# Kernel optimization log

Measured on AMD Instinct MI355X. Metric: run time of the kernel, lower is better.

Reference implementation:

```python
import jax, jax.numpy as jnp
import numpy as np

B, T, C, H, E = 4, 128, 256, 8, 64  # batch, tokens, n_embd, n_head, edge_dim
D = C // H


def setup_inputs() -> dict:
    key = jax.random.key(0)
    ks = jax.random.split(key, 12)
    s = 0.02
    return {
        "x": jax.random.normal(ks[0], (B, T, C), jnp.float32),
        "aux_x": jax.random.normal(ks[1], (B, T, C), jnp.float32),
        "mask": jnp.ones((B, T, T), jnp.int32),
        "edge": jax.random.normal(ks[2], (B, T, T, E), jnp.float32),
        "Wq": jax.random.normal(ks[3], (C, C), jnp.float32) * s,
        "bq": jnp.zeros((C,), jnp.float32),
        "Wk": jax.random.normal(ks[4], (C, C + E), jnp.float32) * s,
        "bk": jnp.zeros((C,), jnp.float32),
        "Wv": jax.random.normal(ks[5], (C, C + E), jnp.float32) * s,
        "bv": jnp.zeros((C,), jnp.float32),
        "Wp": jax.random.normal(ks[6], (C, C), jnp.float32) * s,
        "bp": jnp.zeros((C,), jnp.float32),
    }


def reference(x, aux_x, mask, edge, Wq, bq, Wk, bk, Wv, bv, Wp, bp):
    Bx, Tx, Cx = x.shape
    q = x @ Wq.T + bq  # [B,T,C]
    # per-pair augmented features: node i broadcast over all j, concat edge(i,j)
    aug = jnp.concatenate(
        [jnp.broadcast_to(x[:, :, None, :], (Bx, Tx, Tx, Cx)), edge], axis=-1
    )  # [B,T,T,C+E]
    k = aug @ Wk.T + bk  # [B,T,T,C]
    v = aug @ Wv.T + bv  # [B,T,T,C]
    q = q.reshape(Bx, Tx, H, D).transpose(0, 2, 1, 3)          # [B,H,T,D]
    k = k.reshape(Bx, Tx, Tx, H, D).transpose(0, 3, 1, 2, 4)   # [B,H,T,T,D]
    v = v.reshape(Bx, Tx, Tx, H, D).transpose(0, 3, 1, 2, 4)   # [B,H,T,T,D]
    att = jnp.einsum('bhid,bhijd->bhij', q, k) * (1.0 / jnp.sqrt(jnp.float32(D)))
    att = jnp.where(mask[:, None] == 0, -jnp.inf, att)
    all_masked = (mask == 0).all(-1)[:, None, :, None]  # rows with no valid key
    att = jnp.where(all_masked, 0.0, att)
    fi = jnp.finfo(att.dtype)
    att = jnp.nan_to_num(att, nan=0.0, posinf=fi.max, neginf=fi.min)
    att = jax.nn.softmax(att, axis=-1)
    y = jnp.einsum('bhij,bhijd->bhid', att, v)  # [B,H,T,D]
    y = y.transpose(0, 2, 1, 3).reshape(Bx, Tx, Cx)
    return y @ Wp.T + bp
```

## Files before the change

### kernel.cpp

```cpp
#include <hip/hip_runtime.h>

#define SENT (-3.402823466e38f)

typedef __attribute__((ext_vector_type(8))) short short8;
typedef __attribute__((ext_vector_type(4))) float floatx4;

#define OFF_QKP   0
#define OFF_AGG   131072
#define OFF_VNODE 262144

__device__ __forceinline__ ushort f2b(float f) {
    uint u = __float_as_uint(f);
    u += 0x7FFFu + ((u >> 16) & 1u);
    return (ushort)(u >> 16);
}
__device__ __forceinline__ short8 pk8(float4 a, float4 b) {
    short8 r;
    r[0]=(short)f2b(a.x); r[1]=(short)f2b(a.y); r[2]=(short)f2b(a.z); r[3]=(short)f2b(a.w);
    r[4]=(short)f2b(b.x); r[5]=(short)f2b(b.y); r[6]=(short)f2b(b.z); r[7]=(short)f2b(b.w);
    return r;
}

__global__ __launch_bounds__(256, 4)
void k1_proj(const float* __restrict__ x, const float* __restrict__ Wq,
             const float* __restrict__ Wv, const float* __restrict__ Wk,
             const float* __restrict__ bq, const float* __restrict__ bv,
             float* __restrict__ vnode, ushort* __restrict__ qkp) {
    __shared__ float xL[16][264];
    __shared__ float qls[16][66];
    int tid = threadIdx.x;
    int w = tid >> 6, lane = tid & 63, g = lane >> 4, r = lane & 15;
    int m  = blockIdx.x & 1;
    int ct = (blockIdx.x >> 1) & 3;
    int rt = blockIdx.x >> 3;
    int r0 = rt*16, c0 = ct*64;

    #pragma unroll
    for (int it = 0; it < 4; ++it) {
        int fid = (tid + 256*it)*4;
        int rr = fid >> 8, k = fid & 255;
        *(float4*)&xL[rr][k] = *(const float4*)&x[(size_t)(r0+rr)*256 + k];
    }
    __syncthreads();

    int c = c0 + w*16 + r;
    const float* Wrow = m ? (Wv + (size_t)c*320) : (Wq + (size_t)c*256);
    floatx4 acc = {0.f,0.f,0.f,0.f};
    #pragma unroll
    for (int kt = 0; kt < 8; ++kt) {
        int k0 = kt*32 + g*8;
        short8 af = pk8(*(float4*)&xL[r][k0], *(float4*)&xL[r][k0+4]);
        short8 bf = pk8(*(const float4*)&Wrow[k0], *(const float4*)&Wrow[k0+4]);
        acc = __builtin_amdgcn_mfma_f32_16x16x32_bf16(af, bf, acc, 0,0,0);
    }
    float bb = m ? bv[c] : bq[c];
    if (m) {
        #pragma unroll
        for (int i = 0; i < 4; ++i)
            vnode[(size_t)(r0 + 4*g + i)*256 + c] = acc[i] + bb;
    } else {
        #pragma unroll
        for (int i = 0; i < 4; ++i)
            qls[4*g + i][w*16 + r] = acc[i] + bb;
        __syncthreads();
        int rr = tid >> 4, es = tid & 15;
        int h0 = ct*2;
        float a0[4] = {0,0,0,0}, a1[4] = {0,0,0,0};
        const float* wk0 = Wk + (size_t)(h0*32)*320 + 256 + es*4;
        const float* wk1 = Wk + (size_t)((h0+1)*32)*320 + 256 + es*4;
        #pragma unroll 8
        for (int d = 0; d < 32; ++d) {
            float q0 = qls[rr][d];
            float q1 = qls[rr][32 + d];
            float4 w0 = *(const float4*)&wk0[(size_t)d*320];
            float4 w1 = *(const float4*)&wk1[(size_t)d*320];
            a0[0]+=q0*w0.x; a0[1]+=q0*w0.y; a0[2]+=q0*w0.z; a0[3]+=q0*w0.w;
            a1[0]+=q1*w1.x; a1[1]+=q1*w1.y; a1[2]+=q1*w1.z; a1[3]+=q1*w1.w;
        }
        const float s = 0.17677669529663687f;
        ushort4 u0, u1;
        u0.x=f2b(a0[0]*s); u0.y=f2b(a0[1]*s); u0.z=f2b(a0[2]*s); u0.w=f2b(a0[3]*s);
        u1.x=f2b(a1[0]*s); u1.y=f2b(a1[1]*s); u1.z=f2b(a1[2]*s); u1.w=f2b(a1[3]*s);
        size_t base = (size_t)(r0 + rr)*512;
        *(ushort4*)&qkp[base + h0*64 + es*4]     = u0;
        *(ushort4*)&qkp[base + (h0+1)*64 + es*4] = u1;
    }
}

__global__ __launch_bounds__(512, 4)
void k2_attn(const float* __restrict__ edge, const int* __restrict__ msk,
             const ushort* __restrict__ qkp, ushort* __restrict__ aggO) {
    __shared__ ushort edsA[128][72];
    __shared__ ushort qkpL[16][64];
    __shared__ float  attL[8][132];
    __shared__ ushort attT[16][136];
    __shared__ float  mval[128];
    int tid = threadIdx.x;
    int w = tid >> 6, lane = tid & 63, g = lane >> 4, r = lane & 15;
    int row = blockIdx.x;

    float4 ef[4];
    const float* eg = edge + (size_t)row*8192;
    #pragma unroll
    for (int it = 0; it < 4; ++it)
        ef[it] = *(const float4*)(eg + (size_t)(tid + 512*it)*4);

    if (tid < 256) {
        ushort* qf = (ushort*)qkpL;
        *(uint*)&qf[tid*2]        = *(const uint*)&qkp[(size_t)row*512 + tid*2];
        *(uint*)&qf[512 + tid*2]  = 0u;
    }
    if (tid < 128) mval[tid] = (msk[(size_t)row*128 + tid] != 0) ? 1.0f : 0.0f;
    if (tid < 136) {
        #pragma unroll
        for (int hp = 8; hp < 16; ++hp) attT[hp][tid] = 0;
    }
    #pragma unroll
    for (int it = 0; it < 4; ++it) {
        int fid = (tid + 512*it)*4;
        int j = fid >> 6, e = fid & 63;
        uint lo = (uint)f2b(ef[it].x) | ((uint)f2b(ef[it].y) << 16);
        uint hi = (uint)f2b(ef[it].z) | ((uint)f2b(ef[it].w) << 16);
        *(uint2*)&edsA[j][e] = make_uint2(lo, hi);
    }
    __syncthreads();

    {
        int mt = w;
        floatx4 acc = {0,0,0,0};
        #pragma unroll
        for (int kt = 0; kt < 2; ++kt) {
            short8 af = *(short8*)&edsA[mt*16 + r][kt*32 + g*8];
            short8 bf = *(short8*)&qkpL[r][kt*32 + g*8];
            acc = __builtin_amdgcn_mfma_f32_16x16x32_bf16(af, bf, acc, 0,0,0);
        }
        if (r < 8) {
            #pragma unroll
            for (int i = 0; i < 4; ++i) {
                int j = mt*16 + 4*g + i;
                attL[r][j] = (mval[j] > 0.5f) ? acc[i] : SENT;
            }
        }
    }
    __syncthreads();

    {
        int h = w;
        float v0 = attL[h][lane];
        float v1 = attL[h][64 + lane];
        float mx = fmaxf(v0, v1);
        #pragma unroll
        for (int off = 32; off >= 1; off >>= 1) mx = fmaxf(mx, __shfl_xor(mx, off));
        float e0 = __expf(v0 - mx), e1 = __expf(v1 - mx);
        float smv = e0 + e1;
        #pragma unroll
        for (int off = 32; off >= 1; off >>= 1) smv += __shfl_xor(smv, off);
        float inv = 1.0f / smv;
        attT[h][lane]      = f2b(e0 * inv);
        attT[h][64 + lane] = f2b(e1 * inv);
    }
    __syncthreads();

    if (w < 4) {
        floatx4 acc = {0,0,0,0};
        #pragma unroll
        for (int kt = 0; kt < 4; ++kt) {
            short8 a2 = *(short8*)&attT[r][kt*32 + g*8];
            short8 b2;
            #pragma unroll
            for (int jj = 0; jj < 8; ++jj)
                b2[jj] = (short)edsA[kt*32 + g*8 + jj][w*16 + r];
            acc = __builtin_amdgcn_mfma_f32_16x16x32_bf16(a2, b2, acc, 0,0,0);
        }
        #pragma unroll
        for (int i = 0; i < 4; ++i) {
            int h = 4*g + i;
            if (h < 8)
                aggO[(size_t)row*512 + h*64 + w*16 + r] = f2b(acc[i]);
        }
    }
}

__global__ __launch_bounds__(256, 2)
void k3_out(const float* __restrict__ vnode, const ushort* __restrict__ aggI,
            const float* __restrict__ Wv, const float* __restrict__ Wp,
            const float* __restrict__ bp, float* __restrict__ out) {
    __shared__ ushort yL[16][264];
    int tid = threadIdx.x;
    int w = tid >> 6, lane = tid & 63, g = lane >> 4, r = lane & 15;
    int rt = blockIdx.x >> 2, ob = blockIdx.x & 3;
    int r0 = rt*16, o0 = ob*64;

    {
        #pragma unroll
        for (int pi = 0; pi < 4; ++pi) {
            int p = w*4 + pi, h = p >> 1, ntl = p & 1;
            int c = h*32 + ntl*16 + r;
            floatx4 acc;
            #pragma unroll
            for (int i = 0; i < 4; ++i)
                acc[i] = vnode[(size_t)(r0 + 4*g + i)*256 + c];
            #pragma unroll
            for (int kt = 0; kt < 2; ++kt) {
                short8 af = *(const short8*)&aggI[(size_t)(r0 + r)*512 + h*64 + kt*32 + g*8];
                const float* wr = Wv + (size_t)c*320 + 256 + kt*32 + g*8;
                short8 bf = pk8(*(const float4*)wr, *(const float4*)(wr + 4));
                acc = __builtin_amdgcn_mfma_f32_16x16x32_bf16(af, bf, acc, 0,0,0);
            }
            #pragma unroll
            for (int i = 0; i < 4; ++i)
                yL[4*g + i][c] = f2b(acc[i]);
        }
    }
    __syncthreads();

    {
        int o = o0 + w*16 + r;
        floatx4 acc = {0,0,0,0};
        const float* wr = Wp + (size_t)o*256;
        #pragma unroll
        for (int kt = 0; kt < 8; ++kt) {
            int k0 = kt*32 + g*8;
            short8 af = *(short8*)&yL[r][k0];
            short8 bf = pk8(*(const float4*)&wr[k0], *(const float4*)&wr[k0+4]);
            acc = __builtin_amdgcn_mfma_f32_16x16x32_bf16(af, bf, acc, 0,0,0);
        }
        float bb = bp[o];
        #pragma unroll
        for (int i = 0; i < 4; ++i)
            out[(size_t)(r0 + 4*g + i)*256 + o] = acc[i] + bb;
    }
}

extern "C" void kernel_launch(void* const* d_in, const int* in_sizes, int n_in,
                              void* d_out, int out_size, void* d_ws, size_t ws_size,
                              hipStream_t stream) {
    (void)in_sizes; (void)n_in; (void)out_size; (void)ws_size;
    const float* x    = (const float*)d_in[0];
    const int*   msk  = (const int*)d_in[2];
    const float* edge = (const float*)d_in[3];
    const float* Wq   = (const float*)d_in[4];
    const float* bq   = (const float*)d_in[5];
    const float* Wk   = (const float*)d_in[6];
    const float* Wv   = (const float*)d_in[8];
    const float* bv   = (const float*)d_in[9];
    const float* Wp   = (const float*)d_in[10];
    const float* bp   = (const float*)d_in[11];
    float* out = (float*)d_out;
    float* ws  = (float*)d_ws;

    ushort* qkp   = (ushort*)(ws + OFF_QKP);
    ushort* agg   = (ushort*)(ws + OFF_AGG);
    float*  vnode = ws + OFF_VNODE;

    k1_proj<<<256, 256, 0, stream>>>(x, Wq, Wv, Wk, bq, bv, vnode, qkp);
    k2_attn<<<512, 512, 0, stream>>>(edge, msk, qkp, agg);
    k3_out<<<128, 256, 0, stream>>>(vnode, agg, Wv, Wp, bp, out);
}
```

Measured before the change: 21.38 us.

## Fold Wv into Wp to collapse output stage into one GEMM

Precomputes a combined weight M2 = Wp·Wv (node and edge parts) and a bias b2 = Wp·bv + bp in extra blocks of the first kernel, dropping the separate vnode projection. The output kernel then does a single MFMA GEMM over the concatenated [x, agg] features against M2, with no shared-memory intermediate. This removes the vnode round trip and one GEMM stage, at the cost of a serial fp32 weight-product computation inside k1 each call. Folding the weights in bf16 changes rounding behaviour.

```diff
diff --git a/kernel.cpp b/kernel.cpp
--- a/kernel.cpp
+++ b/kernel.cpp
@@ -7,7 +7,8 @@
 
 #define OFF_QKP   0
 #define OFF_AGG   131072
-#define OFF_VNODE 262144
+#define OFF_M2    262144
+#define OFF_B2    360448
 
 __device__ __forceinline__ ushort f2b(float f) {
     uint u = __float_as_uint(f);
@@ -23,48 +24,47 @@
 
 __global__ __launch_bounds__(256, 4)
 void k1_proj(const float* __restrict__ x, const float* __restrict__ Wq,
-             const float* __restrict__ Wv, const float* __restrict__ Wk,
-             const float* __restrict__ bq, const float* __restrict__ bv,
-             float* __restrict__ vnode, ushort* __restrict__ qkp) {
-    __shared__ float xL[16][264];
-    __shared__ float qls[16][66];
+             const float* __restrict__ bq, const float* __restrict__ Wk,
+             const float* __restrict__ Wv, const float* __restrict__ bv,
+             const float* __restrict__ Wp, const float* __restrict__ bp,
+             ushort* __restrict__ qkp, ushort* __restrict__ M2u,
+             float* __restrict__ b2f) {
+    __shared__ float smem[16*264 + 16*66];
     int tid = threadIdx.x;
-    int w = tid >> 6, lane = tid & 63, g = lane >> 4, r = lane & 15;
-    int m  = blockIdx.x & 1;
-    int ct = (blockIdx.x >> 1) & 3;
-    int rt = blockIdx.x >> 3;
-    int r0 = rt*16, c0 = ct*64;
-
-    #pragma unroll
-    for (int it = 0; it < 4; ++it) {
-        int fid = (tid + 256*it)*4;
-        int rr = fid >> 8, k = fid & 255;
-        *(float4*)&xL[rr][k] = *(const float4*)&x[(size_t)(r0+rr)*256 + k];
-    }
-    __syncthreads();
-
-    int c = c0 + w*16 + r;
-    const float* Wrow = m ? (Wv + (size_t)c*320) : (Wq + (size_t)c*256);
-    floatx4 acc = {0.f,0.f,0.f,0.f};
-    #pragma unroll
-    for (int kt = 0; kt < 8; ++kt) {
-        int k0 = kt*32 + g*8;
-        short8 af = pk8(*(float4*)&xL[r][k0], *(float4*)&xL[r][k0+4]);
-        short8 bf = pk8(*(const float4*)&Wrow[k0], *(const float4*)&Wrow[k0+4]);
-        acc = __builtin_amdgcn_mfma_f32_16x16x32_bf16(af, bf, acc, 0,0,0);
-    }
-    float bb = m ? bv[c] : bq[c];
-    if (m) {
-        #pragma unroll
-        for (int i = 0; i < 4; ++i)
-            vnode[(size_t)(r0 + 4*g + i)*256 + c] = acc[i] + bb;
-    } else {
+    int b = blockIdx.x;
+
+    if (b < 128) {
+        float (*xL)[264] = (float(*)[264])smem;
+        float (*qls)[66] = (float(*)[66])(smem + 16*264);
+        int w = tid >> 6, lane = tid & 63, g = lane >> 4, r = lane & 15;
+        int rt = b >> 2, ct = b & 3;
+        int r0 = rt*16, c0 = ct*64, h0 = ct*2;
+
+        #pragma unroll
+        for (int it = 0; it < 4; ++it) {
+            int fid = (tid + 256*it)*4;
+            int rr = fid >> 8, k = fid & 255;
+            *(float4*)&xL[rr][k] = *(const float4*)&x[(size_t)(r0+rr)*256 + k];
+        }
+        __syncthreads();
+
+        int c = c0 + w*16 + r;
+        const float* Wrow = Wq + (size_t)c*256;
+        floatx4 acc = {0.f,0.f,0.f,0.f};
+        #pragma unroll
+        for (int kt = 0; kt < 8; ++kt) {
+            int k0 = kt*32 + g*8;
+            short8 af = pk8(*(float4*)&xL[r][k0], *(float4*)&xL[r][k0+4]);
+            short8 bf = pk8(*(const float4*)&Wrow[k0], *(const float4*)&Wrow[k0+4]);
+            acc = __builtin_amdgcn_mfma_f32_16x16x32_bf16(af, bf, acc, 0,0,0);
+        }
+        float bb = bq[c];
         #pragma unroll
         for (int i = 0; i < 4; ++i)
             qls[4*g + i][w*16 + r] = acc[i] + bb;
         __syncthreads();
+
         int rr = tid >> 4, es = tid & 15;
-        int h0 = ct*2;
         float a0[4] = {0,0,0,0}, a1[4] = {0,0,0,0};
         const float* wk0 = Wk + (size_t)(h0*32)*320 + 256 + es*4;
         const float* wk1 = Wk + (size_t)((h0+1)*32)*320 + 256 + es*4;
@@ -84,6 +84,53 @@
         size_t base = (size_t)(r0 + rr)*512;
         *(ushort4*)&qkp[base + h0*64 + es*4]     = u0;
         *(ushort4*)&qkp[base + (h0+1)*64 + es*4] = u1;
+
+    } else if (b < 160) {
+        float (*WpL)[256] = (float(*)[256])smem;
+        int ot = b - 128, o0 = ot*8;
+        #pragma unroll
+        for (int it = 0; it < 2; ++it) {
+            int fid = (tid + 256*it)*4;
+            int oo = fid >> 8, cc = fid & 255;
+            *(float4*)&WpL[oo][cc] = *(const float4*)&Wp[(size_t)(o0+oo)*256 + cc];
+        }
+        __syncthreads();
+        {
+            float acc[8] = {0,0,0,0,0,0,0,0};
+            for (int c = 0; c < 256; ++c) {
+                float wv = Wv[(size_t)c*320 + tid];
+                #pragma unroll
+                for (int oo = 0; oo < 8; ++oo)
+                    acc[oo] += wv * WpL[oo][c];
+            }
+            #pragma unroll
+            for (int oo = 0; oo < 8; ++oo)
+                M2u[(size_t)(o0+oo)*768 + tid] = f2b(acc[oo]);
+        }
+        {
+            #pragma unroll
+            for (int hh = 0; hh < 2; ++hh) {
+                int he = hh*256 + tid;
+                int h = he >> 6, e = he & 63;
+                float acc[8] = {0,0,0,0,0,0,0,0};
+                #pragma unroll 8
+                for (int cc = 0; cc < 32; ++cc) {
+                    float wv = Wv[(size_t)(h*32+cc)*320 + 256 + e];
+                    #pragma unroll
+                    for (int oo = 0; oo < 8; ++oo)
+                        acc[oo] += wv * WpL[oo][h*32+cc];
+                }
+                #pragma unroll
+                for (int oo = 0; oo < 8; ++oo)
+                    M2u[(size_t)(o0+oo)*768 + 256 + he] = f2b(acc[oo]);
+            }
+        }
+    } else {
+        float acc = bp[tid];
+        const float* wp = Wp + (size_t)tid*256;
+        #pragma unroll 8
+        for (int c = 0; c < 256; ++c) acc += bv[c] * wp[c];
+        b2f[tid] = acc;
     }
 }
 
@@ -126,18 +173,17 @@
     __syncthreads();
 
     {
-        int mt = w;
         floatx4 acc = {0,0,0,0};
         #pragma unroll
         for (int kt = 0; kt < 2; ++kt) {
-            short8 af = *(short8*)&edsA[mt*16 + r][kt*32 + g*8];
+            short8 af = *(short8*)&edsA[w*16 + r][kt*32 + g*8];
             short8 bf = *(short8*)&qkpL[r][kt*32 + g*8];
             acc = __builtin_amdgcn_mfma_f32_16x16x32_bf16(af, bf, acc, 0,0,0);
         }
         if (r < 8) {
             #pragma unroll
             for (int i = 0; i < 4; ++i) {
-                int j = mt*16 + 4*g + i;
+                int j = w*16 + 4*g + i;
                 attL[r][j] = (mval[j] > 0.5f) ? acc[i] : SENT;
             }
         }
@@ -145,9 +191,8 @@
     __syncthreads();
 
     {
-        int h = w;
-        float v0 = attL[h][lane];
-        float v1 = attL[h][64 + lane];
+        float v0 = attL[w][lane];
+        float v1 = attL[w][64 + lane];
         float mx = fmaxf(v0, v1);
         #pragma unroll
         for (int off = 32; off >= 1; off >>= 1) mx = fmaxf(mx, __shfl_xor(mx, off));
@@ -156,8 +201,8 @@
         #pragma unroll
         for (int off = 32; off >= 1; off >>= 1) smv += __shfl_xor(smv, off);
         float inv = 1.0f / smv;
-        attT[h][lane]      = f2b(e0 * inv);
-        attT[h][64 + lane] = f2b(e1 * inv);
+        attT[w][lane]      = f2b(e0 * inv);
+        attT[w][64 + lane] = f2b(e1 * inv);
     }
     __syncthreads();
 
@@ -181,55 +226,39 @@
     }
 }
 
-__global__ __launch_bounds__(256, 2)
-void k3_out(const float* __restrict__ vnode, const ushort* __restrict__ aggI,
-            const float* __restrict__ Wv, const float* __restrict__ Wp,
-            const float* __restrict__ bp, float* __restrict__ out) {
-    __shared__ ushort yL[16][264];
+__global__ __launch_bounds__(256, 4)
+void k3_out(const float* __restrict__ x, const ushort* __restrict__ agg,
+            const ushort* __restrict__ M2u, const float* __restrict__ b2f,
+            float* __restrict__ out) {
     int tid = threadIdx.x;
     int w = tid >> 6, lane = tid & 63, g = lane >> 4, r = lane & 15;
     int rt = blockIdx.x >> 2, ob = blockIdx.x & 3;
     int r0 = rt*16, o0 = ob*64;
 
-    {
-        #pragma unroll
-        for (int pi = 0; pi < 4; ++pi) {
-            int p = w*4 + pi, h = p >> 1, ntl = p & 1;
-            int c = h*32 + ntl*16 + r;
-            floatx4 acc;
-            #pragma unroll
-            for (int i = 0; i < 4; ++i)
-                acc[i] = vnode[(size_t)(r0 + 4*g + i)*256 + c];
-            #pragma unroll
-            for (int kt = 0; kt < 2; ++kt) {
-                short8 af = *(const short8*)&aggI[(size_t)(r0 + r)*512 + h*64 + kt*32 + g*8];
-                const float* wr = Wv + (size_t)c*320 + 256 + kt*32 + g*8;
-                short8 bf = pk8(*(const float4*)wr, *(const float4*)(wr + 4));
-                acc = __builtin_amdgcn_mfma_f32_16x16x32_bf16(af, bf, acc, 0,0,0);
-            }
-            #pragma unroll
-            for (int i = 0; i < 4; ++i)
-                yL[4*g + i][c] = f2b(acc[i]);
-        }
-    }
-    __syncthreads();
-
-    {
-        int o = o0 + w*16 + r;
-        floatx4 acc = {0,0,0,0};
-        const float* wr = Wp + (size_t)o*256;
-        #pragma unroll
-        for (int kt = 0; kt < 8; ++kt) {
-            int k0 = kt*32 + g*8;
-            short8 af = *(short8*)&yL[r][k0];
-            short8 bf = pk8(*(const float4*)&wr[k0], *(const float4*)&wr[k0+4]);
-            acc = __builtin_amdgcn_mfma_f32_16x16x32_bf16(af, bf, acc, 0,0,0);
-        }
-        float bb = bp[o];
-        #pragma unroll
-        for (int i = 0; i < 4; ++i)
-            out[(size_t)(r0 + 4*g + i)*256 + o] = acc[i] + bb;
-    }
+    int o = o0 + w*16 + r;
+    const ushort* m2row = M2u + (size_t)o*768;
+    const float*  xrow  = x + (size_t)(r0 + r)*256;
+    const ushort* arow  = agg + (size_t)(r0 + r)*512;
+
+    floatx4 acc = {0,0,0,0};
+    #pragma unroll
+    for (int kt = 0; kt < 8; ++kt) {
+        int k0 = kt*32 + g*8;
+        short8 af = pk8(*(const float4*)&xrow[k0], *(const float4*)&xrow[k0+4]);
+        short8 bf = *(const short8*)&m2row[k0];
+        acc = __builtin_amdgcn_mfma_f32_16x16x32_bf16(af, bf, acc, 0,0,0);
+    }
+    #pragma unroll
+    for (int kt = 0; kt < 16; ++kt) {
+        int k0 = kt*32 + g*8;
+        short8 af = *(const short8*)&arow[k0];
+        short8 bf = *(const short8*)&m2row[256 + k0];
+        acc = __builtin_amdgcn_mfma_f32_16x16x32_bf16(af, bf, acc, 0,0,0);
+    }
+    float bb = b2f[o];
+    #pragma unroll
+    for (int i = 0; i < 4; ++i)
+        out[(size_t)(r0 + 4*g + i)*256 + o] = acc[i] + bb;
 }
 
 extern "C" void kernel_launch(void* const* d_in, const int* in_sizes, int n_in,
@@ -249,11 +278,12 @@
     float* out = (float*)d_out;
     float* ws  = (float*)d_ws;
 
-    ushort* qkp   = (ushort*)(ws + OFF_QKP);
-    ushort* agg   = (ushort*)(ws + OFF_AGG);
-    float*  vnode = ws + OFF_VNODE;
-
-    k1_proj<<<256, 256, 0, stream>>>(x, Wq, Wv, Wk, bq, bv, vnode, qkp);
+    ushort* qkp = (ushort*)(ws + OFF_QKP);
+    ushort* agg = (ushort*)(ws + OFF_AGG);
+    ushort* M2u = (ushort*)(ws + OFF_M2);
+    float*  b2f = ws + OFF_B2;
+
+    k1_proj<<<161, 256, 0, stream>>>(x, Wq, bq, Wk, Wv, bv, Wp, bp, qkp, M2u, b2f);
     k2_attn<<<512, 512, 0, stream>>>(edge, msk, qkp, agg);
-    k3_out<<<128, 256, 0, stream>>>(vnode, agg, Wv, Wp, bp, out);
-}
+    k3_out<<<128, 256, 0, stream>>>(x, agg, M2u, b2f, out);
+}
```

Measured after the change: 30.63 us. +43.3%, slower.
